# Performance work log

Measured on AMD Instinct MI355X. Metric: run time of the kernel, lower is better.

The kernel has to match this reference:

```python
import jax, jax.numpy as jnp
import numpy as np

NC, NF = 64, 16
Z_NEAR, Z_FAR = 2.0, 6.0
EPS = 1e-5


def volume_integral(z_vals, sigmas, radiances):
    # z_vals/sigmas: (B,R,Z,1), radiances: (B,R,Z,F)
    d = z_vals[..., 1:, :] - z_vals[..., :-1, :]
    dists = jnp.concatenate([d, d[..., -1:, :]], axis=-2)            # (B,R,Z,1)
    alpha = 1.0 - jnp.exp(-jax.nn.relu(sigmas) * dists)
    alpha_shifted = jnp.concatenate(
        [jnp.ones_like(alpha[..., :1, :]), 1.0 - alpha + 1e-10], axis=-2)
    Ts = jnp.cumprod(alpha_shifted, axis=-2)                         # transmittance
    weights = alpha * Ts[..., :-1, :]                                # (B,R,Z,1)
    rgb = jnp.sum(weights * radiances, axis=-2)                      # (B,R,F)
    depth = jnp.sum(weights * z_vals, axis=-2)                       # (B,R,1)
    return rgb, depth, weights


def sample_pdf(bins, weights, u, eps=EPS):
    # bins: (N, S+1), weights: (N, S), u: (N, Nf) in [0,1)
    weights = weights + eps
    pdf = weights / jnp.sum(weights, -1, keepdims=True)
    cdf = jnp.cumsum(pdf, -1)
    cdf = jnp.concatenate([jnp.zeros_like(cdf[:, :1]), cdf], -1)     # (N, S+1)
    inds = jax.vmap(jnp.searchsorted)(cdf, u)                        # side='left' == torch default
    below = jnp.clip(inds - 1, 0, None)
    above = jnp.minimum(inds, weights.shape[-1])
    cdf_g0 = jnp.take_along_axis(cdf, below, 1)
    cdf_g1 = jnp.take_along_axis(cdf, above, 1)
    bins_g0 = jnp.take_along_axis(bins, below, 1)
    bins_g1 = jnp.take_along_axis(bins, above, 1)
    denom = cdf_g1 - cdf_g0
    denom = jnp.where(denom < eps, 1.0, denom)
    return bins_g0 + (u - cdf_g0) / denom * (bins_g1 - bins_g0)


def _render(ros, rds, w_sigma, w_feat, u):
    B, R, _ = ros.shape

    def rad(pts):
        return pts @ w_sigma, jax.nn.sigmoid(pts @ w_feat)

    # coarse stratified samples (lindisp=False)
    zl = jnp.linspace(0.0, 1.0, NC, dtype=ros.dtype)
    z_vals = Z_NEAR + (Z_FAR - Z_NEAR) * zl                          # (NC,)
    z_vals = jnp.broadcast_to(z_vals[None, None, :, None], (B, R, NC, 1))
    pts = ros[:, :, None, :] + rds[:, :, None, :] * z_vals           # (B,R,NC,3)
    sigma, feats = rad(pts)

    # coarse pass + importance resampling (no grad in original)
    _, _, weights = volume_integral(z_vals, sigma, feats)
    weights = jax.lax.stop_gradient(weights).reshape(B * R, NC)
    t = z_vals.reshape(B * R, NC)
    tm = 0.5 * (t[:, :-1] + t[:, 1:])                                # (N, NC-1)
    t_pdf = sample_pdf(tm, weights[:, 1:-1], u)                      # (N, NF)
    t_pdf = jax.lax.stop_gradient(t_pdf).reshape(B, R, NF)

    pts_fine = ros[:, :, None, :] + rds[:, :, None, :] * t_pdf[..., None]
    pts_all = jnp.concatenate([pts, pts_fine], axis=-2)              # (B,R,NC+NF,3)
    sigma_all, feats_all = rad(pts_all)

    # merge-sort coarse+fine by depth and gather
    z_all = jnp.concatenate([z_vals, t_pdf[..., None]], axis=-2)     # (B,R,Z,1)
    idx = jnp.argsort(z_all, axis=-2)
    z_all = jnp.take_along_axis(z_all, idx, axis=-2)
    sigma_all = jnp.take_along_axis(sigma_all, idx, axis=-2)
    feats_all = jnp.take_along_axis(
        feats_all, jnp.broadcast_to(idx, feats_all.shape), axis=-2)

    rgb, depth, weights = volume_integral(z_all, sigma_all, feats_all)
    return rgb, depth, weights


def setup_inputs() -> dict:
    key = jax.random.key(0)
    k = jax.random.split(key, 5)
    B, R = 8, 16384
    return {
        "ros": jax.random.normal(k[0], (B, R, 3), jnp.float32),
        "rds": jax.random.normal(k[1], (B, R, 3), jnp.float32),
        "w_sigma": jax.random.normal(k[2], (3, 1), jnp.float32),
        "w_feat": jax.random.normal(k[3], (3, 3), jnp.float32),
        "u": jax.random.uniform(k[4], (B * R, NF), jnp.float32),
    }


def reference(ros, rds, w_sigma, w_feat, u):
    return _render(ros, rds, w_sigma, w_feat, u)
```

## Files before the change

kernel.cpp:

```cpp
#include <hip/hip_runtime.h>

#define BLK 64
#define STRIDE 79
#define NCC 64
#define NFF 16
#define NZ  80

__device__ __forceinline__ float fast_rcp(float x) { return __builtin_amdgcn_rcpf(x); }

template<int N>
__device__ __forceinline__ void prefix_mul(float* x) {
#pragma unroll
    for (int c = 0; c < N; c += 8) {
#pragma unroll
        for (int i = 1; i < 8; i++)
            if (c + i < N) x[c + i] *= x[c + i - 1];
    }
    constexpr int G = (N + 7) / 8;
    float t[G];
#pragma unroll
    for (int g = 0; g < G; g++) {
        int e = 8 * g + 7; if (e > N - 1) e = N - 1;
        t[g] = x[e];
    }
#pragma unroll
    for (int sh = 1; sh < G; sh <<= 1) {
#pragma unroll
        for (int g = G - 1; g >= sh; --g) t[g] *= t[g - sh];
    }
#pragma unroll
    for (int g = 1; g < G; g++) {
#pragma unroll
        for (int i = 0; i < 8; i++)
            if (8 * g + i < N) x[8 * g + i] *= t[g - 1];
    }
}

template<int N>
__device__ __forceinline__ void prefix_add(float* x) {
#pragma unroll
    for (int c = 0; c < N; c += 8) {
#pragma unroll
        for (int i = 1; i < 8; i++)
            if (c + i < N) x[c + i] += x[c + i - 1];
    }
    constexpr int G = (N + 7) / 8;
    float t[G];
#pragma unroll
    for (int g = 0; g < G; g++) {
        int e = 8 * g + 7; if (e > N - 1) e = N - 1;
        t[g] = x[e];
    }
#pragma unroll
    for (int sh = 1; sh < G; sh <<= 1) {
#pragma unroll
        for (int g = G - 1; g >= sh; --g) t[g] += t[g - sh];
    }
#pragma unroll
    for (int g = 1; g < G; g++) {
#pragma unroll
        for (int i = 0; i < 8; i++)
            if (8 * g + i < N) x[8 * g + i] += t[g - 1];
    }
}

__global__ void __launch_bounds__(BLK, 2)
VolumeRenderer_16192026706363_kernel(const float* __restrict__ ros,
                                     const float* __restrict__ rds,
                                     const float* __restrict__ w_sigma,
                                     const float* __restrict__ w_feat,
                                     const float* __restrict__ u,
                                     float* __restrict__ out,
                                     int nrays)
{
    __shared__ float lds[BLK * STRIDE];
    const int tid = threadIdx.x;
    const int n = blockIdx.x * BLK + tid;
    float* my = &lds[tid * STRIDE];

    const float LOG2E = 1.4426950408889634f;
    const float NEGL2E = -LOG2E;
    const float DIST = 4.0f / 63.0f;
    const float K1 = -DIST * LOG2E;

    const float4* u4p = reinterpret_cast<const float4*>(u + (size_t)n * 16);
    float4 uq0 = u4p[0], uq1 = u4p[1], uq2 = u4p[2], uq3 = u4p[3];
    const float ro0 = ros[n * 3 + 0], ro1 = ros[n * 3 + 1], ro2 = ros[n * 3 + 2];
    const float rd0 = rds[n * 3 + 0], rd1 = rds[n * 3 + 1], rd2 = rds[n * 3 + 2];
    const float s0 = w_sigma[0], s1 = w_sigma[1], s2 = w_sigma[2];

    const float sgA = ro0 * s0 + ro1 * s1 + ro2 * s2;
    const float sgB = rd0 * s0 + rd1 * s1 + rd2 * s2;
    float fA[3], fB[3];
#pragma unroll
    for (int c = 0; c < 3; c++) {
        fA[c] = ro0 * w_feat[0 * 3 + c] + ro1 * w_feat[1 * 3 + c] + ro2 * w_feat[2 * 3 + c];
        fB[c] = rd0 * w_feat[0 * 3 + c] + rd1 * w_feat[1 * 3 + c] + rd2 * w_feat[2 * 3 + c];
    }

    float g[63];
#pragma unroll
    for (int i = 0; i < 63; i++) {
        float zc = 2.0f + DIST * (float)i;
        float sg = fmaf(sgB, zc, sgA);
        g[i] = exp2f(fmaxf(sg, 0.0f) * K1) + 1e-10f;
    }
    prefix_mul<63>(g);

    float c[63];
    c[0] = 0.0f;
#pragma unroll
    for (int i = 1; i <= 62; i++) c[i] = (g[i - 1] - g[i]) + 1e-5f;
    prefix_add<62>(c + 1);

    my[0] = 0.0f;
#pragma unroll
    for (int i = 1; i <= 62; i++) my[i] = c[i];
    const float S = c[62];
    const float invS = fast_rcp(S);

    float uarr[16];
    uarr[0]=uq0.x; uarr[1]=uq0.y; uarr[2]=uq0.z; uarr[3]=uq0.w;
    uarr[4]=uq1.x; uarr[5]=uq1.y; uarr[6]=uq1.z; uarr[7]=uq1.w;
    uarr[8]=uq2.x; uarr[9]=uq2.y; uarr[10]=uq2.z; uarr[11]=uq2.w;
    uarr[12]=uq3.x; uarr[13]=uq3.y; uarr[14]=uq3.z; uarr[15]=uq3.w;

    float tv[16];
#pragma unroll
    for (int q = 0; q < 16; q++) {
        float uu = uarr[q];
        float us = uu * S;
        int lo = 0, hi = 63;
#pragma unroll
        for (int s = 0; s < 6; s++) {
            int mid = (lo + hi) >> 1;
            bool lt = (my[mid] < us);
            lo = lt ? mid + 1 : lo;
            hi = lt ? hi : mid;
        }
        int ind = lo;
        int below = (ind - 1 > 0) ? ind - 1 : 0;
        int above = (ind < 62) ? ind : 62;
        float c0 = my[below] * invS, c1 = my[above] * invS;
        float b0 = fmaf(DIST, (float)below, 2.0f + 0.5f * DIST);
        float denom = c1 - c0;
        denom = (denom < 1e-5f) ? 1.0f : denom;
        float db = (above > below) ? DIST : 0.0f;
        tv[q] = fmaf((uu - c0) * fast_rcp(denom), db, b0);
    }

#pragma unroll
    for (int k = 2; k <= 16; k <<= 1) {
#pragma unroll
        for (int j = k >> 1; j > 0; j >>= 1) {
#pragma unroll
            for (int i = 0; i < 16; i++) {
                int l = i ^ j;
                if (l > i) {
                    float a = tv[i], b = tv[l];
                    float mn = fminf(a, b), mx = fmaxf(a, b);
                    bool up = ((i & k) == 0);
                    tv[i] = up ? mn : mx;
                    tv[l] = up ? mx : mn;
                }
            }
        }
    }

#pragma unroll
    for (int k = 0; k < 78; k++) my[k] = -1.0f;
#pragma unroll
    for (int j = 0; j < 16; j++) {
        float x = (tv[j] - 2.0f) * 15.75f;
        int L = (int)floorf(x) + 1;
        L = (L < 1) ? 1 : (L > 63 ? 63 : L);
        my[j + L - 1] = tv[j];
    }

    float z[NZ];
    z[0] = 2.0f;
    z[NZ - 1] = 6.0f;
    {
        float fc = 0.0f;
#pragma unroll
        for (int k = 1; k <= 78; k++) {
            float s = my[k - 1];
            bool fine = (s >= 0.0f);
            float zc = fmaf(DIST, (float)k - fc, 2.0f);
            z[k] = fine ? s : zc;
            fc += fine ? 1.0f : 0.0f;
        }
    }

    float pp[NZ];
    float dl = 0.0f;
#pragma unroll
    for (int k = 0; k < NZ; k++) {
        float d;
        if (k < NZ - 1) { d = z[k + 1] - z[k]; dl = d; }
        else d = dl;
        float sg = fmaf(sgB, z[k], sgA);
        pp[k] = exp2f(fmaxf(sg, 0.0f) * (d * NEGL2E)) + 1e-10f;
    }
    prefix_mul<NZ>(pp);

    float a0 = 0.f, a1 = 0.f, a2 = 0.f, ad = 0.f;
    float b0a = 0.f, b1a = 0.f, b2a = 0.f, bda = 0.f;
    float* wptr = out + (size_t)nrays * 4 + (size_t)n * NZ;
#pragma unroll
    for (int gq = 0; gq < 20; gq++) {
        float wq[4];
#pragma unroll
        for (int j = 0; j < 4; j++) {
            int k = 4 * gq + j;
            float prev = (k == 0) ? 1.0f : pp[k - 1];
            float w = prev - pp[k];
            float zk = z[k];
            float e0 = exp2f(fmaf(fB[0], zk, fA[0]) * NEGL2E);
            float e1 = exp2f(fmaf(fB[1], zk, fA[1]) * NEGL2E);
            float e2 = exp2f(fmaf(fB[2], zk, fA[2]) * NEGL2E);
            float f0 = fast_rcp(1.0f + e0);
            float f1 = fast_rcp(1.0f + e1);
            float f2 = fast_rcp(1.0f + e2);
            if (j & 1) {
                b0a = fmaf(w, f0, b0a); b1a = fmaf(w, f1, b1a);
                b2a = fmaf(w, f2, b2a); bda = fmaf(w, zk, bda);
            } else {
                a0 = fmaf(w, f0, a0); a1 = fmaf(w, f1, a1);
                a2 = fmaf(w, f2, a2); ad = fmaf(w, zk, ad);
            }
            wq[j] = w;
        }
        *reinterpret_cast<float4*>(wptr + 4 * gq) =
            make_float4(wq[0], wq[1], wq[2], wq[3]);
    }

    out[(size_t)n * 3 + 0] = a0 + b0a;
    out[(size_t)n * 3 + 1] = a1 + b1a;
    out[(size_t)n * 3 + 2] = a2 + b2a;
    out[(size_t)nrays * 3 + n] = ad + bda;
}

extern "C" void kernel_launch(void* const* d_in, const int* in_sizes, int n_in,
                              void* d_out, int out_size, void* d_ws, size_t ws_size,
                              hipStream_t stream) {
    const float* ros = (const float*)d_in[0];
    const float* rds = (const float*)d_in[1];
    const float* w_sigma = (const float*)d_in[2];
    const float* w_feat = (const float*)d_in[3];
    const float* u = (const float*)d_in[4];
    float* out = (float*)d_out;

    int nrays = in_sizes[0] / 3;
    int grid = nrays / BLK;
    VolumeRenderer_16192026706363_kernel<<<grid, BLK, 0, stream>>>(
        ros, rds, w_sigma, w_feat, u, out, nrays);
}
```

Baseline: 108.2 us.

## Split each ray across four lanes with shuffle-based segmented scans

Instead of one thread per ray, each ray is now handled by a group of four lanes. Each lane covers a quarter of the coarse CDF, a quarter of the fine samples and a quarter of the final composite. Cross-lane prefix products and sums, gathering the fine samples and the final reductions use wave shuffles. Block size goes up and LDS per block goes down. The aim is to cut per-thread register arrays (63- and 80-element) so occupancy rises and more parallelism hides latency. The cost is redundant per-ray loads, repeated bitonic sorts in every lane, and shuffle overhead.

```diff
diff --git a/kernel.cpp b/kernel.cpp
--- a/kernel.cpp
+++ b/kernel.cpp
@@ -1,70 +1,18 @@
 #include <hip/hip_runtime.h>
 
-#define BLK 64
+#define BLK 128
+#define RPB 32
 #define STRIDE 79
-#define NCC 64
-#define NFF 16
 #define NZ  80
 
 __device__ __forceinline__ float fast_rcp(float x) { return __builtin_amdgcn_rcpf(x); }
 
-template<int N>
-__device__ __forceinline__ void prefix_mul(float* x) {
-#pragma unroll
-    for (int c = 0; c < N; c += 8) {
-#pragma unroll
-        for (int i = 1; i < 8; i++)
-            if (c + i < N) x[c + i] *= x[c + i - 1];
-    }
-    constexpr int G = (N + 7) / 8;
-    float t[G];
-#pragma unroll
-    for (int g = 0; g < G; g++) {
-        int e = 8 * g + 7; if (e > N - 1) e = N - 1;
-        t[g] = x[e];
-    }
-#pragma unroll
-    for (int sh = 1; sh < G; sh <<= 1) {
-#pragma unroll
-        for (int g = G - 1; g >= sh; --g) t[g] *= t[g - sh];
-    }
-#pragma unroll
-    for (int g = 1; g < G; g++) {
-#pragma unroll
-        for (int i = 0; i < 8; i++)
-            if (8 * g + i < N) x[8 * g + i] *= t[g - 1];
-    }
+__device__ __forceinline__ void grp_gather4(float v, int gb, float o[4]) {
+    o[0] = __shfl(v, gb + 0); o[1] = __shfl(v, gb + 1);
+    o[2] = __shfl(v, gb + 2); o[3] = __shfl(v, gb + 3);
 }
 
-template<int N>
-__device__ __forceinline__ void prefix_add(float* x) {
-#pragma unroll
-    for (int c = 0; c < N; c += 8) {
-#pragma unroll
-        for (int i = 1; i < 8; i++)
-            if (c + i < N) x[c + i] += x[c + i - 1];
-    }
-    constexpr int G = (N + 7) / 8;
-    float t[G];
-#pragma unroll
-    for (int g = 0; g < G; g++) {
-        int e = 8 * g + 7; if (e > N - 1) e = N - 1;
-        t[g] = x[e];
-    }
-#pragma unroll
-    for (int sh = 1; sh < G; sh <<= 1) {
-#pragma unroll
-        for (int g = G - 1; g >= sh; --g) t[g] += t[g - sh];
-    }
-#pragma unroll
-    for (int g = 1; g < G; g++) {
-#pragma unroll
-        for (int i = 0; i < 8; i++)
-            if (8 * g + i < N) x[8 * g + i] += t[g - 1];
-    }
-}
-
-__global__ void __launch_bounds__(BLK, 2)
+__global__ void __launch_bounds__(BLK, 4)
 VolumeRenderer_16192026706363_kernel(const float* __restrict__ ros,
                                      const float* __restrict__ rds,
                                      const float* __restrict__ w_sigma,
@@ -73,20 +21,23 @@
                                      float* __restrict__ out,
                                      int nrays)
 {
-    __shared__ float lds[BLK * STRIDE];
-    const int tid = threadIdx.x;
-    const int n = blockIdx.x * BLK + tid;
-    float* my = &lds[tid * STRIDE];
-
-    const float LOG2E = 1.4426950408889634f;
+    __shared__ float lds[RPB * STRIDE];
+    const int tid  = threadIdx.x;
+    const int gl   = tid & 3;
+    const int rloc = tid >> 2;
+    const int ray  = blockIdx.x * RPB + rloc;
+    const int wl   = tid & 63;
+    const int gb   = wl & ~3;
+    float* my = &lds[rloc * STRIDE];
+
+    const float LOG2E  = 1.4426950408889634f;
     const float NEGL2E = -LOG2E;
-    const float DIST = 4.0f / 63.0f;
-    const float K1 = -DIST * LOG2E;
-
-    const float4* u4p = reinterpret_cast<const float4*>(u + (size_t)n * 16);
-    float4 uq0 = u4p[0], uq1 = u4p[1], uq2 = u4p[2], uq3 = u4p[3];
-    const float ro0 = ros[n * 3 + 0], ro1 = ros[n * 3 + 1], ro2 = ros[n * 3 + 2];
-    const float rd0 = rds[n * 3 + 0], rd1 = rds[n * 3 + 1], rd2 = rds[n * 3 + 2];
+    const float DIST   = 4.0f / 63.0f;
+    const float K1     = -DIST * LOG2E;
+
+    const float4 uq = *reinterpret_cast<const float4*>(u + (size_t)ray * 16 + gl * 4);
+    const float ro0 = ros[ray * 3 + 0], ro1 = ros[ray * 3 + 1], ro2 = ros[ray * 3 + 2];
+    const float rd0 = rds[ray * 3 + 0], rd1 = rds[ray * 3 + 1], rd2 = rds[ray * 3 + 2];
     const float s0 = w_sigma[0], s1 = w_sigma[1], s2 = w_sigma[2];
 
     const float sgA = ro0 * s0 + ro1 * s1 + ro2 * s2;
@@ -98,37 +49,57 @@
         fB[c] = rd0 * w_feat[0 * 3 + c] + rd1 * w_feat[1 * 3 + c] + rd2 * w_feat[2 * 3 + c];
     }
 
-    float g[63];
-#pragma unroll
-    for (int i = 0; i < 63; i++) {
-        float zc = 2.0f + DIST * (float)i;
-        float sg = fmaf(sgB, zc, sgA);
-        g[i] = exp2f(fmaxf(sg, 0.0f) * K1) + 1e-10f;
-    }
-    prefix_mul<63>(g);
-
-    float c[63];
-    c[0] = 0.0f;
-#pragma unroll
-    for (int i = 1; i <= 62; i++) c[i] = (g[i - 1] - g[i]) + 1e-5f;
-    prefix_add<62>(c + 1);
-
-    my[0] = 0.0f;
-#pragma unroll
-    for (int i = 1; i <= 62; i++) my[i] = c[i];
-    const float S = c[62];
+    const int base = gl * 16;
+    float pl[16];
+    {
+        float p = 1.0f;
+#pragma unroll
+        for (int t = 0; t < 16; t++) {
+            float zc = fmaf(DIST, (float)(base + t), 2.0f);
+            float e = exp2f(fmaxf(fmaf(sgB, zc, sgA), 0.0f) * K1) + 1e-10f;
+            p *= e; pl[t] = p;
+        }
+    }
+    float Ltot = (gl == 3) ? pl[14] : pl[15];
+    float x4[4];
+    grp_gather4(Ltot, gb, x4);
+    const float Eprod = (gl == 0) ? 1.0f : (gl == 1) ? x4[0]
+                      : (gl == 2) ? x4[0] * x4[1] : x4[0] * x4[1] * x4[2];
+
+    float Lsum;
+    {
+        float cs = 0.0f;
+#pragma unroll
+        for (int t = 0; t < 16; t++) {
+            int i = base + t;
+            float plprev = (t == 0) ? 1.0f : pl[t - 1];
+            float w = Eprod * (plprev - pl[t]);
+            if (i >= 1 && i <= 62) cs += w + 1e-5f;
+        }
+        Lsum = cs;
+    }
+    grp_gather4(Lsum, gb, x4);
+    const float Csum0 = (gl == 0) ? 0.0f : (gl == 1) ? x4[0]
+                      : (gl == 2) ? x4[0] + x4[1] : x4[0] + x4[1] + x4[2];
+    const float S = x4[0] + x4[1] + x4[2] + x4[3];
     const float invS = fast_rcp(S);
 
-    float uarr[16];
-    uarr[0]=uq0.x; uarr[1]=uq0.y; uarr[2]=uq0.z; uarr[3]=uq0.w;
-    uarr[4]=uq1.x; uarr[5]=uq1.y; uarr[6]=uq1.z; uarr[7]=uq1.w;
-    uarr[8]=uq2.x; uarr[9]=uq2.y; uarr[10]=uq2.z; uarr[11]=uq2.w;
-    uarr[12]=uq3.x; uarr[13]=uq3.y; uarr[14]=uq3.z; uarr[15]=uq3.w;
-
-    float tv[16];
-#pragma unroll
-    for (int q = 0; q < 16; q++) {
-        float uu = uarr[q];
+    {
+        float cs = 0.0f;
+#pragma unroll
+        for (int t = 0; t < 16; t++) {
+            int i = base + t;
+            float plprev = (t == 0) ? 1.0f : pl[t - 1];
+            float w = Eprod * (plprev - pl[t]);
+            if (i >= 1 && i <= 62) { cs += w + 1e-5f; my[i] = Csum0 + cs; }
+        }
+        if (gl == 0) my[0] = 0.0f;
+    }
+
+    float tv[4];
+#pragma unroll
+    for (int q = 0; q < 4; q++) {
+        float uu = (q == 0) ? uq.x : (q == 1) ? uq.y : (q == 2) ? uq.z : uq.w;
         float us = uu * S;
         int lo = 0, hi = 63;
 #pragma unroll
@@ -149,6 +120,14 @@
         tv[q] = fmaf((uu - c0) * fast_rcp(denom), db, b0);
     }
 
+    float arr[16];
+#pragma unroll
+    for (int k = 0; k < 4; k++) {
+        float g4[4];
+        grp_gather4(tv[k], gb, g4);
+#pragma unroll
+        for (int s = 0; s < 4; s++) arr[s * 4 + k] = g4[s];
+    }
 #pragma unroll
     for (int k = 2; k <= 16; k <<= 1) {
 #pragma unroll
@@ -157,88 +136,119 @@
             for (int i = 0; i < 16; i++) {
                 int l = i ^ j;
                 if (l > i) {
-                    float a = tv[i], b = tv[l];
+                    float a = arr[i], b = arr[l];
                     float mn = fminf(a, b), mx = fmaxf(a, b);
                     bool up = ((i & k) == 0);
-                    tv[i] = up ? mn : mx;
-                    tv[l] = up ? mx : mn;
+                    arr[i] = up ? mn : mx;
+                    arr[l] = up ? mx : mn;
                 }
             }
         }
     }
 
 #pragma unroll
-    for (int k = 0; k < 78; k++) my[k] = -1.0f;
-#pragma unroll
-    for (int j = 0; j < 16; j++) {
-        float x = (tv[j] - 2.0f) * 15.75f;
+    for (int t = 0; t < 20; t++) {
+        int j = gl + 4 * t;
+        if (j < 78) my[j] = -1.0f;
+    }
+#pragma unroll
+    for (int q = 0; q < 4; q++) {
+        int j = gl * 4 + q;
+        float v = arr[j];
+        float x = (v - 2.0f) * 15.75f;
         int L = (int)floorf(x) + 1;
         L = (L < 1) ? 1 : (L > 63 ? 63 : L);
-        my[j + L - 1] = tv[j];
-    }
-
-    float z[NZ];
-    z[0] = 2.0f;
-    z[NZ - 1] = 6.0f;
-    {
-        float fc = 0.0f;
-#pragma unroll
-        for (int k = 1; k <= 78; k++) {
-            float s = my[k - 1];
-            bool fine = (s >= 0.0f);
-            float zc = fmaf(DIST, (float)k - fc, 2.0f);
-            z[k] = fine ? s : zc;
-            fc += fine ? 1.0f : 0.0f;
-        }
-    }
-
-    float pp[NZ];
-    float dl = 0.0f;
-#pragma unroll
-    for (int k = 0; k < NZ; k++) {
-        float d;
-        if (k < NZ - 1) { d = z[k + 1] - z[k]; dl = d; }
-        else d = dl;
-        float sg = fmaf(sgB, z[k], sgA);
-        pp[k] = exp2f(fmaxf(sg, 0.0f) * (d * NEGL2E)) + 1e-10f;
-    }
-    prefix_mul<NZ>(pp);
+        my[j + L - 1] = v;
+    }
+
+    const int sbase = 20 * gl;
+    const int slen = (gl < 3) ? 20 : 18;
+    float sv[20], fl[20];
+    float lt = 0.0f;
+#pragma unroll
+    for (int t = 0; t < 20; t++) {
+        if (t < slen) {
+            sv[t] = my[sbase + t];
+            fl[t] = (sv[t] >= 0.0f) ? 1.0f : 0.0f;
+            lt += fl[t];
+        } else { sv[t] = 0.0f; fl[t] = 0.0f; }
+    }
+    grp_gather4(lt, gb, x4);
+    float fcnt = (gl == 0) ? 0.0f : (gl == 1) ? x4[0]
+               : (gl == 2) ? x4[0] + x4[1] : x4[0] + x4[1] + x4[2];
+
+    float zpos[20];
+#pragma unroll
+    for (int t = 0; t < 20; t++) {
+        if (t < slen) {
+            float zc = fmaf(DIST, (float)(sbase + t + 1) - fcnt, 2.0f);
+            zpos[t] = (fl[t] > 0.0f) ? sv[t] : zc;
+            fcnt += fl[t];
+        } else zpos[t] = 0.0f;
+    }
+    int src = gb + ((gl == 0) ? 0 : gl - 1);
+    float carry = __shfl(zpos[19], src);
+    float myz[20];
+    myz[0] = (gl == 0) ? 2.0f : carry;
+#pragma unroll
+    for (int t = 1; t < 20; t++) {
+        int idx = t - 1;
+        myz[t] = (idx < slen) ? zpos[idx] : 6.0f;
+    }
+
+    float d[20];
+#pragma unroll
+    for (int t = 0; t < 19; t++) d[t] = myz[t + 1] - myz[t];
+    d[19] = (gl < 3) ? (zpos[19] - myz[19]) : d[18];
+
+    float Pl[20];
+    {
+        float p = 1.0f;
+#pragma unroll
+        for (int t = 0; t < 20; t++) {
+            float sg = fmaf(sgB, myz[t], sgA);
+            float e = exp2f(fmaxf(sg, 0.0f) * (d[t] * NEGL2E)) + 1e-10f;
+            p *= e; Pl[t] = p;
+        }
+    }
+    grp_gather4(Pl[19], gb, x4);
+    const float E2 = (gl == 0) ? 1.0f : (gl == 1) ? x4[0]
+                   : (gl == 2) ? x4[0] * x4[1] : x4[0] * x4[1] * x4[2];
 
     float a0 = 0.f, a1 = 0.f, a2 = 0.f, ad = 0.f;
-    float b0a = 0.f, b1a = 0.f, b2a = 0.f, bda = 0.f;
-    float* wptr = out + (size_t)nrays * 4 + (size_t)n * NZ;
-#pragma unroll
-    for (int gq = 0; gq < 20; gq++) {
+    float* wptr = out + (size_t)nrays * 4 + (size_t)ray * NZ + sbase;
+#pragma unroll
+    for (int g5 = 0; g5 < 5; g5++) {
         float wq[4];
 #pragma unroll
         for (int j = 0; j < 4; j++) {
-            int k = 4 * gq + j;
-            float prev = (k == 0) ? 1.0f : pp[k - 1];
-            float w = prev - pp[k];
-            float zk = z[k];
+            int t = 4 * g5 + j;
+            float Tprev = (t == 0) ? E2 : E2 * Pl[t - 1];
+            float w = Tprev - E2 * Pl[t];
+            float zk = myz[t];
             float e0 = exp2f(fmaf(fB[0], zk, fA[0]) * NEGL2E);
             float e1 = exp2f(fmaf(fB[1], zk, fA[1]) * NEGL2E);
             float e2 = exp2f(fmaf(fB[2], zk, fA[2]) * NEGL2E);
-            float f0 = fast_rcp(1.0f + e0);
-            float f1 = fast_rcp(1.0f + e1);
-            float f2 = fast_rcp(1.0f + e2);
-            if (j & 1) {
-                b0a = fmaf(w, f0, b0a); b1a = fmaf(w, f1, b1a);
-                b2a = fmaf(w, f2, b2a); bda = fmaf(w, zk, bda);
-            } else {
-                a0 = fmaf(w, f0, a0); a1 = fmaf(w, f1, a1);
-                a2 = fmaf(w, f2, a2); ad = fmaf(w, zk, ad);
-            }
+            a0 = fmaf(w, fast_rcp(1.0f + e0), a0);
+            a1 = fmaf(w, fast_rcp(1.0f + e1), a1);
+            a2 = fmaf(w, fast_rcp(1.0f + e2), a2);
+            ad = fmaf(w, zk, ad);
             wq[j] = w;
         }
-        *reinterpret_cast<float4*>(wptr + 4 * gq) =
+        *reinterpret_cast<float4*>(wptr + 4 * g5) =
             make_float4(wq[0], wq[1], wq[2], wq[3]);
     }
 
-    out[(size_t)n * 3 + 0] = a0 + b0a;
-    out[(size_t)n * 3 + 1] = a1 + b1a;
-    out[(size_t)n * 3 + 2] = a2 + b2a;
-    out[(size_t)nrays * 3 + n] = ad + bda;
+    a0 += __shfl_xor(a0, 1); a0 += __shfl_xor(a0, 2);
+    a1 += __shfl_xor(a1, 1); a1 += __shfl_xor(a1, 2);
+    a2 += __shfl_xor(a2, 1); a2 += __shfl_xor(a2, 2);
+    ad += __shfl_xor(ad, 1); ad += __shfl_xor(ad, 2);
+    if (gl == 0) {
+        out[(size_t)ray * 3 + 0] = a0;
+        out[(size_t)ray * 3 + 1] = a1;
+        out[(size_t)ray * 3 + 2] = a2;
+        out[(size_t)nrays * 3 + ray] = ad;
+    }
 }
 
 extern "C" void kernel_launch(void* const* d_in, const int* in_sizes, int n_in,
@@ -252,7 +262,7 @@
     float* out = (float*)d_out;
 
     int nrays = in_sizes[0] / 3;
-    int grid = nrays / BLK;
+    int grid = nrays / RPB;
     VolumeRenderer_16192026706363_kernel<<<grid, BLK, 0, stream>>>(
         ros, rds, w_sigma, w_feat, u, out, nrays);
 }
```

After: 102.0 us. -5.7%, faster.
